# Kernel optimization log

Measured on AMD Instinct MI355X. Metric: run time of the kernel, lower is better.

The kernel has to match this reference:

```python
import jax, jax.numpy as jnp
import numpy as np

NQ, NT, NA = 10000, 50000, 50000
E_GR, E_LT, E_SIM, E_COMP, E_GEN = 50000, 50000, 80000, 100000, 50000
HID, NH, HC, DOT, NL = 512, 4, 128, 256, 2
NEG_SLOPE = 0.2  # PyG GATv2Conv default negative_slope


def _gatv2(x_src, x_dst, src, dst, Wl, bl, Wr, br, att, bias, n_dst):
    # GATv2: x_j = lin_l(x_src), x_i = lin_r(x_dst); e = att . leaky_relu(x_i + x_j)
    xl = (x_src @ Wl + bl).reshape(-1, NH, HC)   # [Ns,H,C]
    xr = (x_dst @ Wr + br).reshape(-1, NH, HC)   # [Nd,H,C]
    m = jax.nn.leaky_relu(xl[src] + xr[dst], NEG_SLOPE)      # [E,H,C]
    logits = jnp.einsum('ehc,hc->eh', m, att)                # [E,H]
    lmax = jax.lax.stop_gradient(jax.ops.segment_max(logits, dst, num_segments=n_dst))
    lmax = jnp.where(jnp.isfinite(lmax), lmax, 0.0)
    ex = jnp.exp(logits - lmax[dst])
    denom = jax.ops.segment_sum(ex, dst, num_segments=n_dst)
    alpha = ex / (denom[dst] + 1e-16)                        # softmax over incoming edges
    out = jax.ops.segment_sum(xl[src] * alpha[:, :, None], dst, num_segments=n_dst)
    return out.reshape(n_dst, NH * HC) + bias


def _layernorm(x, g, b):
    mu = x.mean(-1, keepdims=True)
    var = ((x - mu) ** 2).mean(-1, keepdims=True)
    return (x - mu) / jnp.sqrt(var + 1e-5) * g + b


def _forward(xq, xt, xa, answer_features,
             qp_W, qp_b, tp_W, tp_b, ap_W, ap_b,
             afp_W1, afp_b1, afp_W2, afp_b2,
             conv_Wl, conv_bl, conv_Wr, conv_br, conv_att, conv_bias,
             qh_W, qh_b, qh_g, qh_beta, rh_W, rh_b, rh_g, rh_beta, score_bias,
             ei_gr, ei_lt, ei_sim, ei_comp, ei_gen):
    hq = xq @ qp_W + qp_b
    ht = xt @ tp_W + tp_b
    ha = xa @ ap_W + ap_b
    # add_self_loops=True only for ('query','similar_to','query')
    loops = jnp.arange(NQ, dtype=ei_sim.dtype)
    sim_src = jnp.concatenate([ei_sim[0], loops])
    sim_dst = jnp.concatenate([ei_sim[1], loops])
    for l in range(NL):
        P = lambda r: (conv_Wl[l, r], conv_bl[l, r], conv_Wr[l, r], conv_br[l, r], conv_att[l, r], conv_bias[l, r])
        o_gr = _gatv2(hq, ht, ei_gr[0], ei_gr[1], *P(0), NT)          # query -> think
        o_rgr = _gatv2(ht, hq, ei_gr[1], ei_gr[0], *P(1), NQ)         # think -> query (rev)
        o_lt = _gatv2(ht, ha, ei_lt[0], ei_lt[1], *P(2), NA)          # think -> answer
        o_rlt = _gatv2(ha, ht, ei_lt[1], ei_lt[0], *P(3), NT)         # answer -> think (rev)
        o_sim = _gatv2(hq, hq, sim_src, sim_dst, *P(4), NQ)           # query -> query
        o_cmp = _gatv2(ht, ht, ei_comp[0], ei_comp[1], *P(5), NT)     # think -> think
        # HeteroConv aggr='mean' across relations per destination type, then relu
        hq = jax.nn.relu((o_rgr + o_sim) / 2.0)
        ht = jax.nn.relu((o_gr + o_rlt + o_cmp) / 3.0)
        ha = jax.nn.relu(o_lt)
    q_emb = hq[ei_gen[0]]
    a_emb = ha[ei_gen[1]]
    t_emb = ht[ei_gen[1]]  # faithful to source: think indexed with answer-side index
    af_emb = jax.nn.relu(answer_features @ afp_W1 + afp_b1) @ afp_W2 + afp_b2
    q = _layernorm(q_emb @ qh_W + qh_b, qh_g, qh_beta)
    r = _layernorm(jnp.concatenate([t_emb, a_emb, af_emb], -1) @ rh_W + rh_b, rh_g, rh_beta)
    return (q * r).sum(-1) / jnp.sqrt(jnp.float32(DOT)) + score_bias


def setup_inputs() -> dict:
    ks = jax.random.split(jax.random.key(0), 40)
    n = lambda j, shape, s=0.05: jax.random.normal(ks[j], shape, jnp.float32) * s
    ri = lambda j, shape, hi: jax.random.randint(ks[j], shape, 0, hi, jnp.int32)
    return dict(
        xq=n(0, (NQ, 384), 1.0), xt=n(1, (NT, 384), 1.0), xa=n(2, (NA, 384), 1.0),
        answer_features=n(3, (E_GEN, 6), 1.0),
        qp_W=n(4, (384, HID)), qp_b=n(5, (HID,)),
        tp_W=n(6, (384, HID)), tp_b=n(7, (HID,)),
        ap_W=n(8, (384, HID)), ap_b=n(9, (HID,)),
        afp_W1=n(10, (6, 64)), afp_b1=n(11, (64,)),
        afp_W2=n(12, (64, HID)), afp_b2=n(13, (HID,)),
        conv_Wl=n(14, (NL, 6, HID, HID)), conv_bl=n(15, (NL, 6, HID)),
        conv_Wr=n(16, (NL, 6, HID, HID)), conv_br=n(17, (NL, 6, HID)),
        conv_att=n(18, (NL, 6, NH, HC)), conv_bias=n(19, (NL, 6, HID)),
        qh_W=n(20, (HID, DOT)), qh_b=n(21, (DOT,)),
        qh_g=jnp.ones((DOT,), jnp.float32), qh_beta=jnp.zeros((DOT,), jnp.float32),
        rh_W=n(22, (HID * 3, DOT)), rh_b=n(23, (DOT,)),
        rh_g=jnp.ones((DOT,), jnp.float32), rh_beta=jnp.zeros((DOT,), jnp.float32),
        score_bias=jnp.zeros((1,), jnp.float32),
        ei_gr=jnp.stack([ri(24, (E_GR,), NQ), ri(25, (E_GR,), NT)]),
        ei_lt=jnp.stack([ri(26, (E_LT,), NT), ri(27, (E_LT,), NA)]),
        ei_sim=ri(28, (2, E_SIM), NQ),
        ei_comp=ri(29, (2, E_COMP), NT),
        ei_gen=jnp.stack([ri(30, (E_GEN,), NQ), ri(31, (E_GEN,), NA)]),
    )


def reference(xq, xt, xa, answer_features,
              qp_W, qp_b, tp_W, tp_b, ap_W, ap_b,
              afp_W1, afp_b1, afp_W2, afp_b2,
              conv_Wl, conv_bl, conv_Wr, conv_br, conv_att, conv_bias,
              qh_W, qh_b, qh_g, qh_beta, rh_W, rh_b, rh_g, rh_beta, score_bias,
              ei_gr, ei_lt, ei_sim, ei_comp, ei_gen):
    return _forward(xq, xt, xa, answer_features,
                    qp_W, qp_b, tp_W, tp_b, ap_W, ap_b,
                    afp_W1, afp_b1, afp_W2, afp_b2,
                    conv_Wl, conv_bl, conv_Wr, conv_br, conv_att, conv_bias,
                    qh_W, qh_b, qh_g, qh_beta, rh_W, rh_b, rh_g, rh_beta, score_bias,
                    ei_gr, ei_lt, ei_sim, ei_comp, ei_gen)
```

## Files before the change

### kernel.cpp

```cpp
#include <hip/hip_runtime.h>
#include <cstdio>
#include <type_traits>

#define NQ 10000
#define NT 50000
#define NA 50000
#define E_GR 50000
#define E_LT 50000
#define E_SIM 80000
#define E_COMP 100000
#define E_GEN 50000
#define NEG_SLOPE 0.2f

#define NDTOT 220000
#define NSTOT 220000
#define ETOT  390000
__device__ __constant__ const int c_degOff[7]  = {0, 50000, 60000, 110000, 120000, 170000, 220000};
__device__ __constant__ const int c_sOff[7]    = {0, 10000, 60000, 110000, 120000, 170000, 220000};
__device__ __constant__ const int c_eOff[7]    = {0, 50000, 100000, 150000, 240000, 340000, 390000};
__device__ __constant__ const int c_nb[6]      = {49, 10, 49, 10, 49, 49};
__device__ __constant__ const int c_nbOff[7]   = {0, 49, 59, 108, 118, 167, 216};
__device__ __constant__ const int c_snb[6]     = {10, 49, 49, 10, 49, 49};
__device__ __constant__ const int c_snbOff[7]  = {0, 10, 59, 108, 118, 167, 216};

typedef unsigned short bf16_t;
typedef unsigned int u32;
typedef __attribute__((ext_vector_type(8))) short short8v;
typedef __attribute__((ext_vector_type(4))) float f32x4;

__device__ __forceinline__ float bf2f(u32 bits) { return __uint_as_float(bits << 16); }
__device__ __forceinline__ u32 f2bf(float f) {
  u32 u = __float_as_uint(f);
  return (u + 0x7FFFu + ((u >> 16) & 1u)) >> 16;
}
__device__ __forceinline__ u32 pack2(float a, float b) { return f2bf(a) | (f2bf(b) << 16); }
__device__ __forceinline__ void unpack8(uint4 u, float* f) {
  f[0] = bf2f(u.x & 0xffffu); f[1] = bf2f(u.x >> 16);
  f[2] = bf2f(u.y & 0xffffu); f[3] = bf2f(u.y >> 16);
  f[4] = bf2f(u.z & 0xffffu); f[5] = bf2f(u.z >> 16);
  f[6] = bf2f(u.w & 0xffffu); f[7] = bf2f(u.w >> 16);
}

__device__ __forceinline__ void gload16(const void* g, void* l) {
  __builtin_amdgcn_global_load_lds(
      (const __attribute__((address_space(1))) void*)g,
      (__attribute__((address_space(3))) void*)l, 16, 0, 0);
}

template <typename CT>
__global__ __launch_bounds__(512, 4) void bgemm(
    const bf16_t* __restrict__ A0, const bf16_t* __restrict__ Bt0,
    const float* __restrict__ bias0, CT* __restrict__ C0,
    const int* __restrict__ ridx0, int N0, const int* __restrict__ Nc0,
    const bf16_t* __restrict__ A1, const bf16_t* __restrict__ Bt1,
    const float* __restrict__ bias1, CT* __restrict__ C1,
    const int* __restrict__ ridx1, int N1, const int* __restrict__ Nc1,
    int K, int M, int accumulate)
{
  __shared__ short lds[3][12288];
  const int z = blockIdx.z;
  const bf16_t* A   = z ? A1 : A0;
  const bf16_t* Bt  = z ? Bt1 : Bt0;
  const float* bias = z ? bias1 : bias0;
  CT* C             = z ? C1 : C0;
  const int* ridx   = z ? ridx1 : ridx0;
  const int* Nc     = z ? Nc1 : Nc0;
  int N             = z ? N1 : N0;
  if (Nc) N = *Nc;

  const int tid = threadIdx.x;
  const int ncol = gridDim.x;
  const int nband = (N + 127) >> 7;
  int lin = blockIdx.y * ncol + blockIdx.x;
  if (lin >= ncol * nband) return;

  int band, col;
  const int full = (nband >> 3) * 8 * ncol;
  if (lin < full) {
    int g = lin >> 3, x = lin & 7;
    band = x + 8 * (g / ncol);
    col  = g % ncol;
  } else {
    int r = lin - full;
    band = (nband & ~7) + r / ncol;
    col  = r % ncol;
  }
  const int bm = band * 128, bn = col * 256;

  const int lane = tid & 63;
  const int w = tid >> 6;
  const int wr = w >> 2, wc = w & 3;
  const int fr = lane & 15, fg = lane >> 4;

  const int kg = (((tid & 3) ^ ((tid >> 3) & 3)) << 3);
  const int rr = tid >> 2;
  int ra = min(bm + rr, N - 1);
  const bf16_t* gA0 = A + (size_t)(ridx ? ridx[ra] : ra) * K + kg;
  const bf16_t* gB0 = Bt + (size_t)(bn + rr) * K + kg;
  const bf16_t* gB1 = Bt + (size_t)(bn + 128 + rr) * K + kg;
  const int wb = w << 9;

  f32x4 acc[4][4];
#pragma unroll
  for (int i = 0; i < 4; ++i)
#pragma unroll
    for (int j = 0; j < 4; ++j) acc[i][j] = (f32x4){0.f, 0.f, 0.f, 0.f};

  auto stage = [&](int buf, int k0) {
    short* base = &lds[buf][0];
    gload16(gA0 + k0, base + wb);
    gload16(gB0 + k0, base + 4096 + wb);
    gload16(gB1 + k0, base + 8192 + wb);
  };

  const int nsteps = K >> 5;
  stage(0, 0);
  const int co = (fg ^ ((fr >> 1) & 3)) << 3;
  for (int s = 0; s < nsteps; ++s) {
    const int cur = s % 3;
    if (s + 1 < nsteps) {
      stage((s + 1) % 3, (s + 1) << 5);
      asm volatile("s_waitcnt vmcnt(3)" ::: "memory");
    } else {
      asm volatile("s_waitcnt vmcnt(0)" ::: "memory");
    }
    __builtin_amdgcn_s_barrier();
    asm volatile("" ::: "memory");
    const short* LA = &lds[cur][0];
    const short* LB = &lds[cur][4096];
    short8v b[4];
#pragma unroll
    for (int j = 0; j < 4; ++j) {
      int R = wc * 64 + j * 16 + fr;
      b[j] = *(const short8v*)&LB[R * 32 + co];
    }
#pragma unroll
    for (int i = 0; i < 4; ++i) {
      int R = wr * 64 + i * 16 + fr;
      short8v a = *(const short8v*)&LA[R * 32 + co];
#pragma unroll
      for (int j = 0; j < 4; ++j)
        acc[i][j] = __builtin_amdgcn_mfma_f32_16x16x32_bf16(b[j], a,
                                                            acc[i][j], 0, 0, 0);
    }
    asm volatile("" ::: "memory");
  }

  float4 bv[4];
#pragma unroll
  for (int j = 0; j < 4; ++j) {
    bv[j] = make_float4(0.f, 0.f, 0.f, 0.f);
    if (!accumulate && bias)
      bv[j] = *(const float4*)(bias + bn + wc * 64 + j * 16 + fg * 4);
  }
#pragma unroll
  for (int i = 0; i < 4; ++i) {
    const int n = bm + wr * 64 + i * 16 + fr;
    if (n >= N) continue;
#pragma unroll
    for (int j = 0; j < 4; ++j) {
      const int m0 = bn + wc * 64 + j * 16 + fg * 4;
      f32x4 v = acc[i][j];
      if constexpr (std::is_same<CT, float>::value) {
        float* p = C + (size_t)n * M + m0;
        if (accumulate) {
          float4 o = *(float4*)p;
          o.x += v[0]; o.y += v[1]; o.z += v[2]; o.w += v[3];
          *(float4*)p = o;
        } else {
          *(float4*)p = make_float4(v[0] + bv[j].x, v[1] + bv[j].y,
                                    v[2] + bv[j].z, v[3] + bv[j].w);
        }
      } else {
        uint2 o;
        o.x = pack2(v[0] + bv[j].x, v[1] + bv[j].y);
        o.y = pack2(v[2] + bv[j].z, v[3] + bv[j].w);
        *(uint2*)(C + (size_t)n * M + m0) = o;
      }
    }
  }
}

__device__ __forceinline__ void wT_tile(
    const float* __restrict__ W, bf16_t* __restrict__ Wt, int K, int M)
{
  __shared__ float sm[32][33];
  int mb = blockIdx.x * 32, kb = blockIdx.y * 32;
  int tx = threadIdx.x & 31, ty = threadIdx.x >> 5;
#pragma unroll
  for (int i = 0; i < 4; ++i)
    sm[ty + i * 8][tx] = W[(size_t)(kb + ty + i * 8) * M + mb + tx];
  __syncthreads();
#pragma unroll
  for (int i = 0; i < 4; ++i)
    Wt[(size_t)(mb + ty + i * 8) * K + kb + tx] = (bf16_t)f2bf(sm[tx][ty + i * 8]);
}

__global__ __launch_bounds__(256) void convert_wT(
    const float* __restrict__ W, bf16_t* __restrict__ Wt, int K, int M)
{
  wT_tile(W + (size_t)blockIdx.z * K * M, Wt + (size_t)blockIdx.z * K * M, K, M);
}
__global__ __launch_bounds__(256) void convert_wT24(
    const float* __restrict__ Wl, bf16_t* __restrict__ wl,
    const float* __restrict__ Wr, bf16_t* __restrict__ wr)
{
  int z = blockIdx.z;
  size_t o = (size_t)(z < 12 ? z : z - 12) * 512 * 512;
  if (z < 12) wT_tile(Wl + o, wl + o, 512, 512);
  else        wT_tile(Wr + o, wr + o, 512, 512);
}
__global__ __launch_bounds__(256) void convert_wT3(
    const float* __restrict__ W0, const float* __restrict__ W1,
    const float* __restrict__ W2, bf16_t* __restrict__ T0,
    bf16_t* __restrict__ T1, bf16_t* __restrict__ T2)
{
  int z = blockIdx.z;
  const float* W = z == 0 ? W0 : z == 1 ? W1 : W2;
  bf16_t* T = z == 0 ? T0 : z == 1 ? T1 : T2;
  wT_tile(W, T, 384, 512);
}
__global__ __launch_bounds__(256) void convert_wT4h(
    const float* __restrict__ qh, const float* __restrict__ rh,
    bf16_t* __restrict__ wqh, bf16_t* __restrict__ wrh)
{
  int z = blockIdx.z;
  if (z == 0) wT_tile(qh, wqh, 512, 256);
  else        wT_tile(rh + (size_t)(z - 1) * 512 * 256,
                      wrh + (size_t)(z - 1) * 256 * 512, 512, 256);
}

__global__ __launch_bounds__(256) void cast_flat(
    const float* __restrict__ in, bf16_t* __restrict__ out, int n4)
{
  int t = blockIdx.x * 256 + threadIdx.x;
  if (t >= n4) return;
  float4 v = ((const float4*)in)[t];
  uint2 o;
  o.x = pack2(v.x, v.y);
  o.y = pack2(v.z, v.w);
  ((uint2*)out)[t] = o;
}

__global__ __launch_bounds__(256) void fold_cvec(
    const float* __restrict__ b2, const float* __restrict__ rh2,
    float* __restrict__ cvec)
{
  int m = threadIdx.x;
  float s = 0.f;
  for (int k = 0; k < 512; ++k) s = fmaf(b2[k], rh2[(size_t)k * 256 + m], s);
  cvec[m] = s;
}

#define N4_XQ (NQ * 96)
#define N4_XT (NT * 96)
#define N4_XA (NA * 96)
__global__ __launch_bounds__(256) void cast3(
    const float* __restrict__ xq, const float* __restrict__ xt,
    const float* __restrict__ xa, bf16_t* __restrict__ xqb,
    bf16_t* __restrict__ xtb, bf16_t* __restrict__ xab)
{
  long g = (long)blockIdx.x * 256 + threadIdx.x;
  const float* in; bf16_t* out; long idx;
  if (g < N4_XQ)                { in = xq; out = xqb; idx = g; }
  else if (g < N4_XQ + N4_XT)   { in = xt; out = xtb; idx = g - N4_XQ; }
  else if (g < N4_XQ + N4_XT + N4_XA) { in = xa; out = xab; idx = g - N4_XQ - N4_XT; }
  else return;
  float4 v = ((const float4*)in)[idx];
  uint2 o;
  o.x = pack2(v.x, v.y);
  o.y = pack2(v.z, v.w);
  ((uint2*)out)[idx] = o;
}

__global__ __launch_bounds__(256) void combine_bias6(
    const float* __restrict__ cb, float* __restrict__ bcAll)
{
  int g = blockIdx.x * 256 + threadIdx.x;
  if (g >= 6 * 512) return;
  int row = g >> 9, j = g & 511;
  int l = row / 3, kind = row % 3;
  const float* b = cb + (size_t)l * 6 * 512;
  float v;
  if (kind == 0)      v = (b[0 * 512 + j] + b[3 * 512 + j] + b[5 * 512 + j]) / 3.f;
  else if (kind == 1) v = (b[1 * 512 + j] + b[4 * 512 + j]) * 0.5f;
  else                v = b[2 * 512 + j];
  bcAll[(size_t)row * 512 + j] = v;
}

__device__ __forceinline__ int find_rel6(int g, const int* off) {
  int r = 0;
#pragma unroll
  for (int k = 1; k < 6; ++k) r += (g >= off[k]);
  return r;
}

__global__ __launch_bounds__(256) void hist6(
    const int* __restrict__ d0, const int* __restrict__ d1,
    const int* __restrict__ d2, const int* __restrict__ d3,
    const int* __restrict__ d4, const int* __restrict__ d5,
    const int* __restrict__ s0p, const int* __restrict__ s1p,
    const int* __restrict__ s2p, const int* __restrict__ s3p,
    const int* __restrict__ s4p, const int* __restrict__ s5p,
    int* __restrict__ degAll, int* __restrict__ sdegAll, int* __restrict__ pos)
{
  int g = blockIdx.x * 256 + threadIdx.x;
  if (g >= ETOT) return;
  int r = find_rel6(g, c_eOff);
  int le = g - c_eOff[r];
  const int* dp = r == 0 ? d0 : r == 1 ? d1 : r == 2 ? d2 : r == 3 ? d3
                : r == 4 ? d4 : d5;
  const int* sp = r == 0 ? s0p : r == 1 ? s1p : r == 2 ? s2p : r == 3 ? s3p
                : r == 4 ? s4p : s5p;
  pos[g] = atomicAdd(&degAll[c_degOff[r] + dp[le]], 1);
  atomicAdd(&sdegAll[c_sOff[r] + sp[le]], 1);
}

template <int PRED, int SRC>
__global__ __launch_bounds__(256) void scan1_6(
    const int* __restrict__ in, int* __restrict__ out, int* __restrict__ bsum)
{
  __shared__ int sm[256];
  int b = blockIdx.x;
  const int* nbOff = SRC ? c_snbOff : c_nbOff;
  const int* dOff  = SRC ? c_sOff : c_degOff;
  int r = 0;
#pragma unroll
  for (int k = 1; k < 6; ++k) r += (b >= nbOff[k]);
  int lb = b - nbOff[r];
  int base0 = dOff[r], n = dOff[r + 1] - base0;
  int t = threadIdx.x;
  int base = lb * 1024 + t * 4;
  int v[4], sum = 0;
#pragma unroll
  for (int k = 0; k < 4; ++k) {
    int raw = (base + k < n) ? in[base0 + base + k] : 0;
    v[k] = PRED == 0 ? raw : PRED == 1 ? (raw >= 2 ? 1 : 0) : (raw >= 1 ? 1 : 0);
    sum += v[k];
  }
  sm[t] = sum;
  __syncthreads();
  for (int off = 1; off < 256; off <<= 1) {
    int x = (t >= off) ? sm[t - off] : 0;
    __syncthreads();
    sm[t] += x;
    __syncthreads();
  }
  int run = (t > 0) ? sm[t - 1] : 0;
  if (t == 255) bsum[r * 64 + lb] = sm[255];
#pragma unroll
  for (int k = 0; k < 4; ++k) {
    if (base + k < n) out[base0 + base + k] = run;
    run += v[k];
  }
}

template <int SRC>
__global__ __launch_bounds__(64) void scan2_6(
    int* __restrict__ bsum, int* __restrict__ total)
{
  __shared__ int sm[64];
  int r = blockIdx.x;
  int nb = SRC ? c_snb[r] : c_nb[r];
  int t = threadIdx.x;
  int v = (t < nb) ? bsum[r * 64 + t] : 0;
  sm[t] = v;
  __syncthreads();
  for (int off = 1; off < 64; off <<= 1) {
    int x = (t >= off) ? sm[t - off] : 0;
    __syncthreads();
    sm[t] += x;
    __syncthreads();
  }
  if (t < nb) bsum[r * 64 + t] = sm[t] - v;
  if (total && t == nb - 1) total[r] = sm[t];
}

template <int SRC>
__global__ __launch_bounds__(256) void scan3_6(
    int* __restrict__ out, const int* __restrict__ bsum)
{
  int g = blockIdx.x * 256 + threadIdx.x;
  if (g >= (SRC ? NSTOT : NDTOT)) return;
  const int* dOff = SRC ? c_sOff : c_degOff;
  int r = find_rel6(g, dOff);
  int ln = g - dOff[r];
  out[g] += bsum[r * 64 + (ln >> 10)];
}

__global__ __launch_bounds__(256) void scatter6(
    const int* __restrict__ d0, const int* __restrict__ d1,
    const int* __restrict__ d2, const int* __restrict__ d3,
    const int* __restrict__ d4, const int* __restrict__ d5,
    const int* __restrict__ s0p, const int* __restrict__ s1p,
    const int* __restrict__ s2p, const int* __restrict__ s3p,
    const int* __restrict__ s4p, const int* __restrict__ s5p,
    const int* __restrict__ startAll, const int* __restrict__ pos,
    const int* __restrict__ sposAll,
    int* __restrict__ eidxAll, int* __restrict__ srcCAll)
{
  int g = blockIdx.x * 256 + threadIdx.x;
  if (g >= ETOT) return;
  int r = find_rel6(g, c_eOff);
  int le = g - c_eOff[r];
  const int* dp = r == 0 ? d0 : r == 1 ? d1 : r == 2 ? d2 : r == 3 ? d3
                : r == 4 ? d4 : d5;
  const int* sp = r == 0 ? s0p : r == 1 ? s1p : r == 2 ? s2p : r == 3 ? s3p
                : r == 4 ? s4p : s5p;
  eidxAll[c_eOff[r] + startAll[c_degOff[r] + dp[le]] + pos[g]] = le;
  srcCAll[g] = sposAll[c_sOff[r] + sp[le]];
}

template <int SRC, int THR>
__global__ __launch_bounds__(256) void compact6(
    const int* __restrict__ degA, const int* __restrict__ cposA,
    int* __restrict__ cidxA)
{
  int g = blockIdx.x * 256 + threadIdx.x;
  if (g >= (SRC ? NSTOT : NDTOT)) return;
  if (degA[g] >= THR) {
    const int* dOff = SRC ? c_sOff : c_degOff;
    int r = find_rel6(g, dOff);
    cidxA[dOff[r] + cposA[g]] = g - dOff[r];
  }
}

__global__ __launch_bounds__(256) void gat_fused(
    const bf16_t* __restrict__ xl, const bf16_t* __restrict__ xr,
    const int* __restrict__ srcC, const int* __restrict__ start,
    const int* __restrict__ deg, const int* __restrict__ eidx,
    const int* __restrict__ cpos, const float* __restrict__ att,
    bf16_t* __restrict__ acc, int Nd, int accumulate,
    const float* __restrict__ bc, float inv_div)
{
  int d = blockIdx.x * 4 + (threadIdx.x >> 6);
  if (d >= Nd) return;
  int lane = threadIdx.x & 63;

  float acc8[8] = {0.f, 0.f, 0.f, 0.f, 0.f, 0.f, 0.f, 0.f};
  int n = deg[d], s0 = start[d];
  if (n == 1) {
    int s = srcC[eidx[s0]];
    unpack8(*(const uint4*)(xl + (size_t)s * 512 + lane * 8), acc8);
  } else if (n > 1) {
    float xrr[8];
    unpack8(*(const uint4*)(xr + (size_t)cpos[d] * 512 + lane * 8), xrr);
    float at[8];
    *(float4*)(at)     = *(const float4*)(att + lane * 8);
    *(float4*)(at + 4) = *(const float4*)(att + lane * 8 + 4);
    float den = 0.f;
    int sN = srcC[eidx[s0]];
    for (int i = 0; i < n; ++i) {
      int s = sN;
      if (i + 1 < n) sN = srcC[eidx[s0 + i + 1]];
      float f[8];
      unpack8(*(const uint4*)(xl + (size_t)s * 512 + lane * 8), f);
      float p = 0.f;
#pragma unroll
      for (int k = 0; k < 8; ++k) {
        float x = f[k] + xrr[k];
        p = fmaf(at[k], x >= 0.f ? x : NEG_SLOPE * x, p);
      }
#pragma unroll
      for (int m = 8; m >= 1; m >>= 1) p += __shfl_xor(p, m);
      float ex = __expf(p);
      den += ex;
#pragma unroll
      for (int k = 0; k < 8; ++k) acc8[k] = fmaf(ex, f[k], acc8[k]);
    }
    float inv = 1.f / (den + 1e-16f);
#pragma unroll
    for (int k = 0; k < 8; ++k) acc8[k] *= inv;
  }

  bf16_t* out = acc + (size_t)d * 512 + lane * 8;
  if (accumulate) {
    float old[8];
    unpack8(*(const uint4*)out, old);
#pragma unroll
    for (int k = 0; k < 8; ++k) acc8[k] += old[k];
  }
  if (bc) {
    float bcv[8];
    *(float4*)(bcv)     = *(const float4*)(bc + lane * 8);
    *(float4*)(bcv + 4) = *(const float4*)(bc + lane * 8 + 4);
#pragma unroll
    for (int k = 0; k < 8; ++k)
      acc8[k] = fmaxf(fmaf(acc8[k], inv_div, bcv[k]), 0.f);
  }
  uint4 s;
  s.x = pack2(acc8[0], acc8[1]); s.y = pack2(acc8[2], acc8[3]);
  s.z = pack2(acc8[4], acc8[5]); s.w = pack2(acc8[6], acc8[7]);
  *(uint4*)out = s;
}

__global__ __launch_bounds__(256) void af_hidden(
    const float* __restrict__ af, const float* __restrict__ W1,
    const float* __restrict__ b1, bf16_t* __restrict__ out, int n)
{
  int t = blockIdx.x * blockDim.x + threadIdx.x;
  if (t >= n * 64) return;
  int i = t >> 6, j = t & 63;
  const float* a = af + (size_t)i * 6;
  float s = b1[j];
#pragma unroll
  for (int k = 0; k < 6; ++k) s = fmaf(a[k], W1[k * 64 + j], s);
  out[t] = (bf16_t)f2bf(fmaxf(s, 0.f));
}

__global__ __launch_bounds__(256) void build_sim(
    const int* __restrict__ ei, int* __restrict__ ss, int* __restrict__ sd)
{
  int t = blockIdx.x * blockDim.x + threadIdx.x;
  if (t >= E_SIM + NQ) return;
  if (t < E_SIM) { ss[t] = ei[t]; sd[t] = ei[E_SIM + t]; }
  else           { ss[t] = t - E_SIM; sd[t] = t - E_SIM; }
}

__global__ __launch_bounds__(256) void head_final(
    const float* __restrict__ qn, const float* __restrict__ rn,
    const float* __restrict__ afr, const float* __restrict__ cvec,
    const int* __restrict__ gsrc, const int* __restrict__ gdst,
    const float* __restrict__ qg, const float* __restrict__ qb,
    const float* __restrict__ rg, const float* __restrict__ rb,
    const float* __restrict__ score_bias, float* __restrict__ out, int E)
{
  int e = blockIdx.x * 4 + (threadIdx.x >> 6);
  if (e >= E) return;
  int lane = threadIdx.x & 63;

  float4 q = *(const float4*)(qn + (size_t)gsrc[e] * 256 + lane * 4);
  float s = q.x + q.y + q.z + q.w;
#pragma unroll
  for (int m = 32; m >= 1; m >>= 1) s += __shfl_xor(s, m);
  float mu = s * (1.f / 256.f);
  float dq0 = q.x - mu, dq1 = q.y - mu, dq2 = q.z - mu, dq3 = q.w - mu;
  float v = dq0 * dq0 + dq1 * dq1 + dq2 * dq2 + dq3 * dq3;
#pragma unroll
  for (int m = 32; m >= 1; m >>= 1) v += __shfl_xor(v, m);
  float rstd = rsqrtf(v * (1.f / 256.f) + 1e-5f);
  float4 g4 = *(const float4*)(qg + lane * 4);
  float4 b4 = *(const float4*)(qb + lane * 4);
  float qn0 = dq0 * rstd * g4.x + b4.x, qn1 = dq1 * rstd * g4.y + b4.y;
  float qn2 = dq2 * rstd * g4.z + b4.z, qn3 = dq3 * rstd * g4.w + b4.w;

  float4 r0 = *(const float4*)(rn + (size_t)gdst[e] * 256 + lane * 4);
  float4 r1 = *(const float4*)(afr + (size_t)e * 256 + lane * 4);
  float4 cv = *(const float4*)(cvec + lane * 4);
  float4 r;
  r.x = r0.x + r1.x + cv.x;
  r.y = r0.y + r1.y + cv.y;
  r.z = r0.z + r1.z + cv.z;
  r.w = r0.w + r1.w + cv.w;
  s = r.x + r.y + r.z + r.w;
#pragma unroll
  for (int m = 32; m >= 1; m >>= 1) s += __shfl_xor(s, m);
  mu = s * (1.f / 256.f);
  float dr0 = r.x - mu, dr1 = r.y - mu, dr2 = r.z - mu, dr3 = r.w - mu;
  v = dr0 * dr0 + dr1 * dr1 + dr2 * dr2 + dr3 * dr3;
#pragma unroll
  for (int m = 32; m >= 1; m >>= 1) v += __shfl_xor(v, m);
  rstd = rsqrtf(v * (1.f / 256.f) + 1e-5f);
  g4 = *(const float4*)(rg + lane * 4);
  b4 = *(const float4*)(rb + lane * 4);
  float rn0 = dr0 * rstd * g4.x + b4.x, rn1 = dr1 * rstd * g4.y + b4.y;
  float rn2 = dr2 * rstd * g4.z + b4.z, rn3 = dr3 * rstd * g4.w + b4.w;

  float d = qn0 * rn0 + qn1 * rn1 + qn2 * rn2 + qn3 * rn3;
#pragma unroll
  for (int m = 32; m >= 1; m >>= 1) d += __shfl_xor(d, m);
  if (lane == 0) out[e] = d * 0.0625f + score_bias[0];
}

extern "C" void kernel_launch(void* const* d_in, const int* in_sizes, int n_in,
                              void* d_out, int out_size, void* d_ws, size_t ws_size,
                              hipStream_t stream) {
  (void)in_sizes; (void)n_in; (void)out_size;
  const float* xq      = (const float*)d_in[0];
  const float* xt      = (const float*)d_in[1];
  const float* xa      = (const float*)d_in[2];
  const float* af      = (const float*)d_in[3];
  const float* qp_W    = (const float*)d_in[4];
  const float* qp_b    = (const float*)d_in[5];
  const float* tp_W    = (const float*)d_in[6];
  const float* tp_b    = (const float*)d_in[7];
  const float* ap_W    = (const float*)d_in[8];
  const float* ap_b    = (const float*)d_in[9];
  const float* afp_W1  = (const float*)d_in[10];
  const float* afp_b1  = (const float*)d_in[11];
  const float* afp_W2  = (const float*)d_in[12];
  const float* afp_b2  = (const float*)d_in[13];
  const float* conv_Wl = (const float*)d_in[14];
  const float* conv_bl = (const float*)d_in[15];
  const float* conv_Wr = (const float*)d_in[16];
  const float* conv_br = (const float*)d_in[17];
  const float* conv_att  = (const float*)d_in[18];
  const float* conv_bias = (const float*)d_in[19];
  const float* qh_W    = (const float*)d_in[20];
  const float* qh_b    = (const float*)d_in[21];
  const float* qh_g    = (const float*)d_in[22];
  const float* qh_beta = (const float*)d_in[23];
  const float* rh_W    = (const float*)d_in[24];
  const float* rh_b    = (const float*)d_in[25];
  const float* rh_g    = (const float*)d_in[26];
  const float* rh_beta = (const float*)d_in[27];
  const float* score_b = (const float*)d_in[28];
  const int* ei_gr   = (const int*)d_in[29];
  const int* ei_lt   = (const int*)d_in[30];
  const int* ei_sim  = (const int*)d_in[31];
  const int* ei_comp = (const int*)d_in[32];
  const int* ei_gen  = (const int*)d_in[33];

  char* base = (char*)d_ws;
  size_t off = 0;
  auto alloc = [&](size_t bytes) {
    void* p = base + off;
    off = (off + bytes + 255) & ~(size_t)255;
    return p;
  };
  bf16_t* hq   = (bf16_t*)alloc((size_t)NQ * 512 * 2);
  bf16_t* ht   = (bf16_t*)alloc((size_t)NT * 512 * 2);
  bf16_t* ha   = (bf16_t*)alloc((size_t)NA * 512 * 2);
  bf16_t* acct = (bf16_t*)alloc((size_t)NT * 512 * 2);
  bf16_t* accq = (bf16_t*)alloc((size_t)NQ * 512 * 2);
  bf16_t* xlb  = (bf16_t*)alloc((size_t)50000 * 512 * 2);
  bf16_t* xrb  = (bf16_t*)alloc((size_t)50000 * 512 * 2);
  int* simsrc  = (int*)alloc((size_t)(E_SIM + NQ) * 4);
  int* simdst  = (int*)alloc((size_t)(E_SIM + NQ) * 4);

  bf16_t* wqp  = (bf16_t*)alloc((size_t)512 * 384 * 2);
  bf16_t* wtp  = (bf16_t*)alloc((size_t)512 * 384 * 2);
  bf16_t* wap  = (bf16_t*)alloc((size_t)512 * 384 * 2);
  bf16_t* wl   = (bf16_t*)alloc((size_t)12 * 512 * 512 * 2);
  bf16_t* wr   = (bf16_t*)alloc((size_t)12 * 512 * 512 * 2);
  bf16_t* wqh  = (bf16_t*)alloc((size_t)256 * 512 * 2);
  bf16_t* wrh0 = (bf16_t*)alloc((size_t)256 * 512 * 2);
  bf16_t* wrh1 = (bf16_t*)alloc((size_t)256 * 512 * 2);
  bf16_t* wrh2 = (bf16_t*)alloc((size_t)256 * 512 * 2);
  float* bcAll = (float*)alloc(6 * 512 * 4);
  bf16_t* a2b    = (bf16_t*)alloc((size_t)64 * 512 * 2);
  float*  wfoldF = (float*)alloc((size_t)64 * 256 * 4);
  bf16_t* wfoldT = (bf16_t*)alloc((size_t)256 * 64 * 2);
  float*  cvec   = (float*)alloc(256 * 4);

  int* degAll   = (int*)alloc((size_t)NDTOT * 4);
  int* startAll = (int*)alloc((size_t)NDTOT * 4);
  int* cposAll  = (int*)alloc((size_t)NDTOT * 4);
  int* cidxAll  = (int*)alloc((size_t)NDTOT * 4);
  int* sdegAll  = (int*)alloc((size_t)NSTOT * 4);
  int* sposAll  = (int*)alloc((size_t)NSTOT * 4);
  int* sidxAll  = (int*)alloc((size_t)NSTOT * 4);
  int* eidxAll  = (int*)alloc((size_t)ETOT * 4);
  int* srcCAll  = (int*)alloc((size_t)ETOT * 4);
  int* posb     = (int*)alloc((size_t)ETOT * 4);
  int* bsum     = (int*)alloc(6 * 64 * 4);
  int* bsum2    = (int*)alloc(6 * 64 * 4);
  int* sbsum    = (int*)alloc(6 * 64 * 4);
  int* ccount   = (int*)alloc(6 * 4);
  int* scount   = (int*)alloc(6 * 4);
  if (off > ws_size) {
    fprintf(stderr, "kernel_launch: ws too small, need %zu have %zu\n", off, ws_size);
    return;
  }

  const int degOff[6] = {0, 50000, 60000, 110000, 120000, 170000};
  const int sOff[6]   = {0, 10000, 60000, 110000, 120000, 170000};
  const int eOff[6]   = {0, 50000, 100000, 150000, 240000, 340000};

  auto gemm1 = [&](const bf16_t* A, const bf16_t* Bt, const float* bias, bf16_t* C,
                   int N_, int K_, int M_, const int* ridx = nullptr) {
    dim3 g(M_ / 256, (N_ + 127) / 128, 1);
    bgemm<bf16_t><<<g, 512, 0, stream>>>(A, Bt, bias, C, ridx, N_, nullptr,
                                         A, Bt, bias, C, ridx, N_, nullptr,
                                         K_, M_, 0);
  };
  auto gemmf1 = [&](const bf16_t* A, const bf16_t* Bt, const float* bias, float* C,
                    int N_, int K_, int M_, int acc_, const int* ridx = nullptr) {
    dim3 g(M_ / 256, (N_ + 127) / 128, 1);
    bgemm<float><<<g, 512, 0, stream>>>(A, Bt, bias, C, ridx, N_, nullptr,
                                        A, Bt, bias, C, ridx, N_, nullptr,
                                        K_, M_, acc_);
  };
  auto gemm2 = [&](const bf16_t* A0, const bf16_t* B0, const float* b0, bf16_t* C0, int N0_,
                   const bf16_t* A1, const bf16_t* B1, const float* b1, bf16_t* C1, int N1_,
                   int K_, int M_) {
    int nb0 = (N0_ + 127) / 128, nb1 = (N1_ + 127) / 128;
    dim3 g(M_ / 256, nb0 > nb1 ? nb0 : nb1, 2);
    bgemm<bf16_t><<<g, 512, 0, stream>>>(A0, B0, b0, C0, nullptr, N0_, nullptr,
                                         A1, B1, b1, C1, nullptr, N1_, nullptr,
                                         K_, M_, 0);
  };
  auto gemm2cc = [&](const bf16_t* A0, const bf16_t* B0, const float* b0, bf16_t* C0,
                     const int* sidx, int N0max, const int* Ns_,
                     const bf16_t* A1, const bf16_t* B1, const float* b1, bf16_t* C1,
                     const int* cidx, int N1max, const int* Ncnt) {
    int nb0 = (N0max + 127) / 128, nb1 = (N1max + 127) / 128;
    dim3 g(2, nb0 > nb1 ? nb0 : nb1, 2);
    bgemm<bf16_t><<<g, 512, 0, stream>>>(A0, B0, b0, C0, sidx, N0max, Ns_,
                                         A1, B1, b1, C1, cidx, N1max, Ncnt,
                                         512, 512, 0);
  };
  auto gemmf2 = [&](const bf16_t* A0, const bf16_t* B0, const float* b0, float* C0, int N0_,
                    const bf16_t* A1, const bf16_t* B1, const float* b1, float* C1, int N1_,
                    int K_, int M_) {
    int nb0 = (N0_ + 127) / 128, nb1 = (N1_ + 127) / 128;
    dim3 g(M_ / 256, nb0 > nb1 ? nb0 : nb1, 2);
    bgemm<float><<<g, 512, 0, stream>>>(A0, B0, b0, C0, nullptr, N0_, nullptr,
                                        A1, B1, b1, C1, nullptr, N1_, nullptr,
                                        K_, M_, 0);
  };

  convert_wT24<<<dim3(16, 16, 24), 256, 0, stream>>>(conv_Wl, wl, conv_Wr, wr);
  convert_wT3<<<dim3(16, 12, 3), 256, 0, stream>>>(qp_W, tp_W, ap_W, wqp, wtp, wap);
  convert_wT4h<<<dim3(8, 16, 4), 256, 0, stream>>>(qh_W, rh_W, wqh, wrh0);
  combine_bias6<<<(6 * 512 + 255) / 256, 256, 0, stream>>>(conv_bias, bcAll);
  cast_flat<<<(64 * 512 / 4 + 255) / 256, 256, 0, stream>>>(afp_W2, a2b, 64 * 512 / 4);
  gemmf1(a2b, wrh2, nullptr, wfoldF, 64, 512, 256, 0);
  convert_wT<<<dim3(8, 2, 1), 256, 0, stream>>>(wfoldF, wfoldT, 64, 256);
  fold_cvec<<<1, 256, 0, stream>>>(afp_b2, rh_W + 1024 * 256, cvec);

  build_sim<<<(E_SIM + NQ + 255) / 256, 256, 0, stream>>>(ei_sim, simsrc, simdst);
  const int* dsts[6]  = {ei_gr + E_GR, ei_gr, ei_lt, simdst,
                         ei_comp + E_COMP, ei_lt + E_LT};
  const int* srcsA[6] = {ei_gr, ei_gr + E_GR, ei_lt + E_LT, simsrc,
                         ei_comp, ei_lt};
  hipMemsetAsync(degAll, 0, (size_t)NDTOT * 4, stream);
  hipMemsetAsync(sdegAll, 0, (size_t)NSTOT * 4, stream);
  hist6<<<(ETOT + 255) / 256, 256, 0, stream>>>(
      dsts[0], dsts[1], dsts[2], dsts[3], dsts[4], dsts[5],
      srcsA[0], srcsA[1], srcsA[2], srcsA[3], srcsA[4], srcsA[5],
      degAll, sdegAll, posb);
  scan1_6<0, 0><<<216, 256, 0, stream>>>(degAll, startAll, bsum);
  scan1_6<1, 0><<<216, 256, 0, stream>>>(degAll, cposAll, bsum2);
  scan1_6<2, 1><<<216, 256, 0, stream>>>(sdegAll, sposAll, sbsum);
  scan2_6<0><<<6, 64, 0, stream>>>(bsum, nullptr);
  scan2_6<0><<<6, 64, 0, stream>>>(bsum2, ccount);
  scan2_6<1><<<6, 64, 0, stream>>>(sbsum, scount);
  scan3_6<0><<<(NDTOT + 255) / 256, 256, 0, stream>>>(startAll, bsum);
  scan3_6<0><<<(NDTOT + 255) / 256, 256, 0, stream>>>(cposAll, bsum2);
  scan3_6<1><<<(NSTOT + 255) / 256, 256, 0, stream>>>(sposAll, sbsum);
  scatter6<<<(ETOT + 255) / 256, 256, 0, stream>>>(
      dsts[0], dsts[1], dsts[2], dsts[3], dsts[4], dsts[5],
      srcsA[0], srcsA[1], srcsA[2], srcsA[3], srcsA[4], srcsA[5],
      startAll, posb, sposAll, eidxAll, srcCAll);
  compact6<0, 2><<<(NDTOT + 255) / 256, 256, 0, stream>>>(degAll, cposAll, cidxAll);
  compact6<1, 1><<<(NSTOT + 255) / 256, 256, 0, stream>>>(sdegAll, sposAll, sidxAll);

  cast3<<<((long)(N4_XQ + N4_XT + N4_XA) + 255) / 256, 256, 0, stream>>>(
      xq, xt, xa, accq, xlb, xrb);
  gemm1(accq, wqp, qp_b, hq, NQ, 384, 512);
  gemm2(xlb, wtp, tp_b, ht, NT, xrb, wap, ap_b, ha, NA, 384, 512);

  const int NdArr[6] = {NT, NQ, NT, NQ, NT, NA};
  const int NsArr[6] = {NQ, NT, NA, NQ, NT, NT};
  bf16_t *hq_i = hq, *ht_i = ht, *hq_o = accq, *ht_o = acct;
  for (int l = 0; l < 2; ++l) {
    const float* bc_t = bcAll + (size_t)(l * 3 + 0) * 512;
    const float* bc_q = bcAll + (size_t)(l * 3 + 1) * 512;
    const float* bc_a = bcAll + (size_t)(l * 3 + 2) * 512;

    struct Rel { const bf16_t* xs; const bf16_t* xd; int po; bf16_t* acc;
                 int accum; const float* bc; float inv; };
    Rel rels[6] = {
      {hq_i, ht_i, 0, ht_o, 0, nullptr, 0.f},
      {ht_i, hq_i, 1, hq_o, 0, nullptr, 0.f},
      {ha,   ht_i, 3, ht_o, 1, nullptr, 0.f},
      {hq_i, hq_i, 4, hq_o, 1, bc_q, 0.5f},
      {ht_i, ht_i, 5, ht_o, 1, bc_t, 1.f / 3.f},
      {ht_i, ha,   2, ha,   0, bc_a, 1.f},
    };
    for (int r = 0; r < 6; ++r) {
      const Rel& R = rels[r];
      int Nd_ = NdArr[r];
      size_t po = (size_t)l * 6 + R.po;
      gemm2cc(R.xs, wl + po * 512 * 512, conv_bl + po * 512, xlb,
              sidxAll + sOff[r], NsArr[r], scount + r,
              R.xd, wr + po * 512 * 512, conv_br + po * 512, xrb,
              cidxAll + degOff[r], Nd_, ccount + r);
      int gb = (Nd_ + 3) / 4;
      gat_fused<<<gb, 256, 0, stream>>>(xlb, xrb, srcCAll + eOff[r],
                                        startAll + degOff[r], degAll + degOff[r],
                                        eidxAll + eOff[r], cposAll + degOff[r],
                                        conv_att + po * 512,
                                        R.acc, Nd_, R.accum, R.bc, R.inv);
    }
    bf16_t* t;
    t = hq_i; hq_i = hq_o; hq_o = t;
    t = ht_i; ht_i = ht_o; ht_o = t;
  }

  float* qn  = (float*)accq;
  float* rn  = (float*)acct;
  float* afr = (float*)xrb;
  bf16_t* afh = xlb;
  const int* gsrc = ei_gen;
  const int* gdst = ei_gen + E_GEN;

  gemmf2(hq_i, wqh, qh_b, qn, NQ, ht_i, wrh0, rh_b, rn, NT, 512, 256);
  gemmf1(ha, wrh1, nullptr, rn, NA, 512, 256, 1);
  af_hidden<<<(E_GEN * 64 + 255) / 256, 256, 0, stream>>>(af, afp_W1, afp_b1,
                                                          afh, E_GEN);
  gemmf1(afh, wfoldT, nullptr, afr, E_GEN, 64, 256, 0);
  head_final<<<(E_GEN + 3) / 4, 256, 0, stream>>>(
      qn, rn, afr, cvec, gsrc, gdst,
      qh_g, qh_beta, rh_g, rh_beta, score_b, (float*)d_out, E_GEN);
}
```

Before: 1.207 ms.

## Cut kernel launches: single-pass scans, merged compaction, batched GEMMs

The three-kernel block scans are replaced by one kernel of 18 blocks, each scanning a whole relation segment serially with a running carry. The two compaction kernels become one, the two degree memsets become one, and the GEMM kernel now takes up to three descriptors so that the projection GEMMs and the head GEMMs are batched into fewer launches. The goal is to cut launch count and small-kernel overhead. The cost is a long serial scan in only 18 blocks, which may take longer than the parallel version for segments of 50k elements.

New measurement: 1.255 ms. 1.04x slower.

```diff
diff --git a/kernel.cpp b/kernel.cpp
--- a/kernel.cpp
+++ b/kernel.cpp
@@ -18,10 +18,6 @@
 __device__ __constant__ const int c_degOff[7]  = {0, 50000, 60000, 110000, 120000, 170000, 220000};
 __device__ __constant__ const int c_sOff[7]    = {0, 10000, 60000, 110000, 120000, 170000, 220000};
 __device__ __constant__ const int c_eOff[7]    = {0, 50000, 100000, 150000, 240000, 340000, 390000};
-__device__ __constant__ const int c_nb[6]      = {49, 10, 49, 10, 49, 49};
-__device__ __constant__ const int c_nbOff[7]   = {0, 49, 59, 108, 118, 167, 216};
-__device__ __constant__ const int c_snb[6]     = {10, 49, 49, 10, 49, 49};
-__device__ __constant__ const int c_snbOff[7]  = {0, 10, 59, 108, 118, 167, 216};
 
 typedef unsigned short bf16_t;
 typedef unsigned int u32;
@@ -47,26 +43,20 @@
       (__attribute__((address_space(3))) void*)l, 16, 0, 0);
 }
 
+struct GemmDesc {
+  const bf16_t* A; const bf16_t* Bt; const float* bias; void* C;
+  const int* ridx; int N; const int* Nc; int K;
+};
+
 template <typename CT>
 __global__ __launch_bounds__(512, 4) void bgemm(
-    const bf16_t* __restrict__ A0, const bf16_t* __restrict__ Bt0,
-    const float* __restrict__ bias0, CT* __restrict__ C0,
-    const int* __restrict__ ridx0, int N0, const int* __restrict__ Nc0,
-    const bf16_t* __restrict__ A1, const bf16_t* __restrict__ Bt1,
-    const float* __restrict__ bias1, CT* __restrict__ C1,
-    const int* __restrict__ ridx1, int N1, const int* __restrict__ Nc1,
-    int K, int M, int accumulate)
+    GemmDesc d0, GemmDesc d1, GemmDesc d2, int M, int accumulate)
 {
   __shared__ short lds[3][12288];
   const int z = blockIdx.z;
-  const bf16_t* A   = z ? A1 : A0;
-  const bf16_t* Bt  = z ? Bt1 : Bt0;
-  const float* bias = z ? bias1 : bias0;
-  CT* C             = z ? C1 : C0;
-  const int* ridx   = z ? ridx1 : ridx0;
-  const int* Nc     = z ? Nc1 : Nc0;
-  int N             = z ? N1 : N0;
-  if (Nc) N = *Nc;
+  GemmDesc d = (z == 2) ? d2 : (z == 1) ? d1 : d0;
+  int N = d.Nc ? *d.Nc : d.N;
+  const int K = d.K;
 
   const int tid = threadIdx.x;
   const int ncol = gridDim.x;
@@ -95,9 +85,9 @@
   const int kg = (((tid & 3) ^ ((tid >> 3) & 3)) << 3);
   const int rr = tid >> 2;
   int ra = min(bm + rr, N - 1);
-  const bf16_t* gA0 = A + (size_t)(ridx ? ridx[ra] : ra) * K + kg;
-  const bf16_t* gB0 = Bt + (size_t)(bn + rr) * K + kg;
-  const bf16_t* gB1 = Bt + (size_t)(bn + 128 + rr) * K + kg;
+  const bf16_t* gA0 = d.A + (size_t)(d.ridx ? d.ridx[ra] : ra) * K + kg;
+  const bf16_t* gB0 = d.Bt + (size_t)(bn + rr) * K + kg;
+  const bf16_t* gB1 = d.Bt + (size_t)(bn + 128 + rr) * K + kg;
   const int wb = w << 9;
 
   f32x4 acc[4][4];
@@ -146,12 +136,13 @@
     asm volatile("" ::: "memory");
   }
 
+  CT* C = (CT*)d.C;
   float4 bv[4];
 #pragma unroll
   for (int j = 0; j < 4; ++j) {
     bv[j] = make_float4(0.f, 0.f, 0.f, 0.f);
-    if (!accumulate && bias)
-      bv[j] = *(const float4*)(bias + bn + wc * 64 + j * 16 + fg * 4);
+    if (!accumulate && d.bias)
+      bv[j] = *(const float4*)(d.bias + bn + wc * 64 + j * 16 + fg * 4);
   }
 #pragma unroll
   for (int i = 0; i < 4; ++i) {
@@ -316,76 +307,50 @@
   atomicAdd(&sdegAll[c_sOff[r] + sp[le]], 1);
 }
 
-template <int PRED, int SRC>
-__global__ __launch_bounds__(256) void scan1_6(
-    const int* __restrict__ in, int* __restrict__ out, int* __restrict__ bsum)
+__global__ __launch_bounds__(256) void scanAll(
+    const int* __restrict__ degAll, const int* __restrict__ sdegAll,
+    int* __restrict__ startAll, int* __restrict__ cposAll,
+    int* __restrict__ sposAll, int* __restrict__ ccount, int* __restrict__ scount)
 {
   __shared__ int sm[256];
   int b = blockIdx.x;
-  const int* nbOff = SRC ? c_snbOff : c_nbOff;
-  const int* dOff  = SRC ? c_sOff : c_degOff;
-  int r = 0;
-#pragma unroll
-  for (int k = 1; k < 6; ++k) r += (b >= nbOff[k]);
-  int lb = b - nbOff[r];
+  int j = b / 6, r = b % 6;
+  const int* dOff = (j == 2) ? c_sOff : c_degOff;
+  const int* in   = (j == 2) ? sdegAll : degAll;
+  int* out = j == 0 ? startAll : j == 1 ? cposAll : sposAll;
   int base0 = dOff[r], n = dOff[r + 1] - base0;
   int t = threadIdx.x;
-  int base = lb * 1024 + t * 4;
-  int v[4], sum = 0;
-#pragma unroll
-  for (int k = 0; k < 4; ++k) {
-    int raw = (base + k < n) ? in[base0 + base + k] : 0;
-    v[k] = PRED == 0 ? raw : PRED == 1 ? (raw >= 2 ? 1 : 0) : (raw >= 1 ? 1 : 0);
-    sum += v[k];
-  }
-  sm[t] = sum;
-  __syncthreads();
-  for (int off = 1; off < 256; off <<= 1) {
-    int x = (t >= off) ? sm[t - off] : 0;
+  int carry = 0;
+  for (int c0 = 0; c0 < n; c0 += 1024) {
+    int base = c0 + t * 4;
+    int v[4], sum = 0;
+#pragma unroll
+    for (int k = 0; k < 4; ++k) {
+      int raw = (base + k < n) ? in[base0 + base + k] : 0;
+      v[k] = j == 0 ? raw : j == 1 ? (raw >= 2 ? 1 : 0) : (raw >= 1 ? 1 : 0);
+      sum += v[k];
+    }
+    sm[t] = sum;
     __syncthreads();
-    sm[t] += x;
+    for (int off = 1; off < 256; off <<= 1) {
+      int x = (t >= off) ? sm[t - off] : 0;
+      __syncthreads();
+      sm[t] += x;
+      __syncthreads();
+    }
+    int run = carry + (t > 0 ? sm[t - 1] : 0);
+#pragma unroll
+    for (int k = 0; k < 4; ++k) {
+      if (base + k < n) out[base0 + base + k] = run;
+      run += v[k];
+    }
+    carry += sm[255];
     __syncthreads();
   }
-  int run = (t > 0) ? sm[t - 1] : 0;
-  if (t == 255) bsum[r * 64 + lb] = sm[255];
-#pragma unroll
-  for (int k = 0; k < 4; ++k) {
-    if (base + k < n) out[base0 + base + k] = run;
-    run += v[k];
-  }
-}
-
-template <int SRC>
-__global__ __launch_bounds__(64) void scan2_6(
-    int* __restrict__ bsum, int* __restrict__ total)
-{
-  __shared__ int sm[64];
-  int r = blockIdx.x;
-  int nb = SRC ? c_snb[r] : c_nb[r];
-  int t = threadIdx.x;
-  int v = (t < nb) ? bsum[r * 64 + t] : 0;
-  sm[t] = v;
-  __syncthreads();
-  for (int off = 1; off < 64; off <<= 1) {
-    int x = (t >= off) ? sm[t - off] : 0;
-    __syncthreads();
-    sm[t] += x;
-    __syncthreads();
-  }
-  if (t < nb) bsum[r * 64 + t] = sm[t] - v;
-  if (total && t == nb - 1) total[r] = sm[t];
-}
-
-template <int SRC>
-__global__ __launch_bounds__(256) void scan3_6(
-    int* __restrict__ out, const int* __restrict__ bsum)
-{
-  int g = blockIdx.x * 256 + threadIdx.x;
-  if (g >= (SRC ? NSTOT : NDTOT)) return;
-  const int* dOff = SRC ? c_sOff : c_degOff;
-  int r = find_rel6(g, dOff);
-  int ln = g - dOff[r];
-  out[g] += bsum[r * 64 + (ln >> 10)];
+  if (t == 0) {
+    if (j == 1) ccount[r] = carry;
+    if (j == 2) scount[r] = carry;
+  }
 }
 
 __global__ __launch_bounds__(256) void scatter6(
@@ -411,17 +376,24 @@
   srcCAll[g] = sposAll[c_sOff[r] + sp[le]];
 }
 
-template <int SRC, int THR>
-__global__ __launch_bounds__(256) void compact6(
-    const int* __restrict__ degA, const int* __restrict__ cposA,
-    int* __restrict__ cidxA)
+__global__ __launch_bounds__(256) void compactBoth(
+    const int* __restrict__ degAll, const int* __restrict__ cposAll,
+    int* __restrict__ cidxAll,
+    const int* __restrict__ sdegAll, const int* __restrict__ sposAll,
+    int* __restrict__ sidxAll)
 {
   int g = blockIdx.x * 256 + threadIdx.x;
-  if (g >= (SRC ? NSTOT : NDTOT)) return;
-  if (degA[g] >= THR) {
-    const int* dOff = SRC ? c_sOff : c_degOff;
-    int r = find_rel6(g, dOff);
-    cidxA[dOff[r] + cposA[g]] = g - dOff[r];
+  if (g < NDTOT) {
+    if (degAll[g] >= 2) {
+      int r = find_rel6(g, c_degOff);
+      cidxAll[c_degOff[r] + cposAll[g]] = g - c_degOff[r];
+    }
+  } else if (g < NDTOT + NSTOT) {
+    int h = g - NDTOT;
+    if (sdegAll[h] >= 1) {
+      int r = find_rel6(h, c_sOff);
+      sidxAll[c_sOff[r] + sposAll[h]] = h - c_sOff[r];
+    }
   }
 }
 
@@ -644,18 +616,15 @@
   float*  cvec   = (float*)alloc(256 * 4);
 
   int* degAll   = (int*)alloc((size_t)NDTOT * 4);
+  int* sdegAll  = (int*)alloc((size_t)NSTOT * 4);
   int* startAll = (int*)alloc((size_t)NDTOT * 4);
   int* cposAll  = (int*)alloc((size_t)NDTOT * 4);
   int* cidxAll  = (int*)alloc((size_t)NDTOT * 4);
-  int* sdegAll  = (int*)alloc((size_t)NSTOT * 4);
   int* sposAll  = (int*)alloc((size_t)NSTOT * 4);
   int* sidxAll  = (int*)alloc((size_t)NSTOT * 4);
   int* eidxAll  = (int*)alloc((size_t)ETOT * 4);
   int* srcCAll  = (int*)alloc((size_t)ETOT * 4);
   int* posb     = (int*)alloc((size_t)ETOT * 4);
-  int* bsum     = (int*)alloc(6 * 64 * 4);
-  int* bsum2    = (int*)alloc(6 * 64 * 4);
-  int* sbsum    = (int*)alloc(6 * 64 * 4);
   int* ccount   = (int*)alloc(6 * 4);
   int* scount   = (int*)alloc(6 * 4);
   if (off > ws_size) {
@@ -667,47 +636,22 @@
   const int sOff[6]   = {0, 10000, 60000, 110000, 120000, 170000};
   const int eOff[6]   = {0, 50000, 100000, 150000, 240000, 340000};
 
-  auto gemm1 = [&](const bf16_t* A, const bf16_t* Bt, const float* bias, bf16_t* C,
-                   int N_, int K_, int M_, const int* ridx = nullptr) {
-    dim3 g(M_ / 256, (N_ + 127) / 128, 1);
-    bgemm<bf16_t><<<g, 512, 0, stream>>>(A, Bt, bias, C, ridx, N_, nullptr,
-                                         A, Bt, bias, C, ridx, N_, nullptr,
-                                         K_, M_, 0);
+  auto mkDesc = [](const bf16_t* A, const bf16_t* Bt, const float* bias, void* C,
+                   const int* ridx, int N, const int* Nc, int K) {
+    GemmDesc d; d.A = A; d.Bt = Bt; d.bias = bias; d.C = C;
+    d.ridx = ridx; d.N = N; d.Nc = Nc; d.K = K; return d;
   };
-  auto gemmf1 = [&](const bf16_t* A, const bf16_t* Bt, const float* bias, float* C,
-                    int N_, int K_, int M_, int acc_, const int* ridx = nullptr) {
-    dim3 g(M_ / 256, (N_ + 127) / 128, 1);
-    bgemm<float><<<g, 512, 0, stream>>>(A, Bt, bias, C, ridx, N_, nullptr,
-                                        A, Bt, bias, C, ridx, N_, nullptr,
-                                        K_, M_, acc_);
+  GemmDesc dz = mkDesc(nullptr, nullptr, nullptr, nullptr, nullptr, 0, nullptr, 32);
+
+  auto launch_b = [&](GemmDesc a, GemmDesc b, GemmDesc c, int nz, int maxN,
+                      int M, int acc_) {
+    dim3 g(M / 256, (maxN + 127) / 128, nz);
+    bgemm<bf16_t><<<g, 512, 0, stream>>>(a, b, c, M, acc_);
   };
-  auto gemm2 = [&](const bf16_t* A0, const bf16_t* B0, const float* b0, bf16_t* C0, int N0_,
-                   const bf16_t* A1, const bf16_t* B1, const float* b1, bf16_t* C1, int N1_,
-                   int K_, int M_) {
-    int nb0 = (N0_ + 127) / 128, nb1 = (N1_ + 127) / 128;
-    dim3 g(M_ / 256, nb0 > nb1 ? nb0 : nb1, 2);
-    bgemm<bf16_t><<<g, 512, 0, stream>>>(A0, B0, b0, C0, nullptr, N0_, nullptr,
-                                         A1, B1, b1, C1, nullptr, N1_, nullptr,
-                                         K_, M_, 0);
-  };
-  auto gemm2cc = [&](const bf16_t* A0, const bf16_t* B0, const float* b0, bf16_t* C0,
-                     const int* sidx, int N0max, const int* Ns_,
-                     const bf16_t* A1, const bf16_t* B1, const float* b1, bf16_t* C1,
-                     const int* cidx, int N1max, const int* Ncnt) {
-    int nb0 = (N0max + 127) / 128, nb1 = (N1max + 127) / 128;
-    dim3 g(2, nb0 > nb1 ? nb0 : nb1, 2);
-    bgemm<bf16_t><<<g, 512, 0, stream>>>(A0, B0, b0, C0, sidx, N0max, Ns_,
-                                         A1, B1, b1, C1, cidx, N1max, Ncnt,
-                                         512, 512, 0);
-  };
-  auto gemmf2 = [&](const bf16_t* A0, const bf16_t* B0, const float* b0, float* C0, int N0_,
-                    const bf16_t* A1, const bf16_t* B1, const float* b1, float* C1, int N1_,
-                    int K_, int M_) {
-    int nb0 = (N0_ + 127) / 128, nb1 = (N1_ + 127) / 128;
-    dim3 g(M_ / 256, nb0 > nb1 ? nb0 : nb1, 2);
-    bgemm<float><<<g, 512, 0, stream>>>(A0, B0, b0, C0, nullptr, N0_, nullptr,
-                                        A1, B1, b1, C1, nullptr, N1_, nullptr,
-                                        K_, M_, 0);
+  auto launch_f = [&](GemmDesc a, GemmDesc b, GemmDesc c, int nz, int maxN,
+                      int M, int acc_) {
+    dim3 g(M / 256, (maxN + 127) / 128, nz);
+    bgemm<float><<<g, 512, 0, stream>>>(a, b, c, M, acc_);
   };
 
   convert_wT24<<<dim3(16, 16, 24), 256, 0, stream>>>(conv_Wl, wl, conv_Wr, wr);
@@ -715,7 +659,8 @@
   convert_wT4h<<<dim3(8, 16, 4), 256, 0, stream>>>(qh_W, rh_W, wqh, wrh0);
   combine_bias6<<<(6 * 512 + 255) / 256, 256, 0, stream>>>(conv_bias, bcAll);
   cast_flat<<<(64 * 512 / 4 + 255) / 256, 256, 0, stream>>>(afp_W2, a2b, 64 * 512 / 4);
-  gemmf1(a2b, wrh2, nullptr, wfoldF, 64, 512, 256, 0);
+  launch_f(mkDesc(a2b, wrh2, nullptr, wfoldF, nullptr, 64, nullptr, 512),
+           dz, dz, 1, 64, 256, 0);
   convert_wT<<<dim3(8, 2, 1), 256, 0, stream>>>(wfoldF, wfoldT, 64, 256);
   fold_cvec<<<1, 256, 0, stream>>>(afp_b2, rh_W + 1024 * 256, cvec);
 
@@ -724,32 +669,26 @@
                          ei_comp + E_COMP, ei_lt + E_LT};
   const int* srcsA[6] = {ei_gr, ei_gr + E_GR, ei_lt + E_LT, simsrc,
                          ei_comp, ei_lt};
-  hipMemsetAsync(degAll, 0, (size_t)NDTOT * 4, stream);
-  hipMemsetAsync(sdegAll, 0, (size_t)NSTOT * 4, stream);
+  hipMemsetAsync(degAll, 0, (size_t)(sdegAll + NSTOT) - (size_t)degAll, stream);
   hist6<<<(ETOT + 255) / 256, 256, 0, stream>>>(
       dsts[0], dsts[1], dsts[2], dsts[3], dsts[4], dsts[5],
       srcsA[0], srcsA[1], srcsA[2], srcsA[3], srcsA[4], srcsA[5],
       degAll, sdegAll, posb);
-  scan1_6<0, 0><<<216, 256, 0, stream>>>(degAll, startAll, bsum);
-  scan1_6<1, 0><<<216, 256, 0, stream>>>(degAll, cposAll, bsum2);
-  scan1_6<2, 1><<<216, 256, 0, stream>>>(sdegAll, sposAll, sbsum);
-  scan2_6<0><<<6, 64, 0, stream>>>(bsum, nullptr);
-  scan2_6<0><<<6, 64, 0, stream>>>(bsum2, ccount);
-  scan2_6<1><<<6, 64, 0, stream>>>(sbsum, scount);
-  scan3_6<0><<<(NDTOT + 255) / 256, 256, 0, stream>>>(startAll, bsum);
-  scan3_6<0><<<(NDTOT + 255) / 256, 256, 0, stream>>>(cposAll, bsum2);
-  scan3_6<1><<<(NSTOT + 255) / 256, 256, 0, stream>>>(sposAll, sbsum);
+  scanAll<<<18, 256, 0, stream>>>(degAll, sdegAll, startAll, cposAll, sposAll,
+                                  ccount, scount);
   scatter6<<<(ETOT + 255) / 256, 256, 0, stream>>>(
       dsts[0], dsts[1], dsts[2], dsts[3], dsts[4], dsts[5],
       srcsA[0], srcsA[1], srcsA[2], srcsA[3], srcsA[4], srcsA[5],
       startAll, posb, sposAll, eidxAll, srcCAll);
-  compact6<0, 2><<<(NDTOT + 255) / 256, 256, 0, stream>>>(degAll, cposAll, cidxAll);
-  compact6<1, 1><<<(NSTOT + 255) / 256, 256, 0, stream>>>(sdegAll, sposAll, sidxAll);
+  compactBoth<<<(NDTOT + NSTOT + 255) / 256, 256, 0, stream>>>(
+      degAll, cposAll, cidxAll, sdegAll, sposAll, sidxAll);
 
   cast3<<<((long)(N4_XQ + N4_XT + N4_XA) + 255) / 256, 256, 0, stream>>>(
       xq, xt, xa, accq, xlb, xrb);
-  gemm1(accq, wqp, qp_b, hq, NQ, 384, 512);
-  gemm2(xlb, wtp, tp_b, ht, NT, xrb, wap, ap_b, ha, NA, 384, 512);
+  launch_b(mkDesc(accq, wqp, qp_b, hq, nullptr, NQ, nullptr, 384),
+           mkDesc(xlb, wtp, tp_b, ht, nullptr, NT, nullptr, 384),
+           mkDesc(xrb, wap, ap_b, ha, nullptr, NA, nullptr, 384),
+           3, NT, 512, 0);
 
   const int NdArr[6] = {NT, NQ, NT, NQ, NT, NA};
   const int NsArr[6] = {NQ, NT, NA, NQ, NT, NT};
@@ -773,10 +712,12 @@
       const Rel& R = rels[r];
       int Nd_ = NdArr[r];
       size_t po = (size_t)l * 6 + R.po;
-      gemm2cc(R.xs, wl + po * 512 * 512, conv_bl + po * 512, xlb,
-              sidxAll + sOff[r], NsArr[r], scount + r,
-              R.xd, wr + po * 512 * 512, conv_br + po * 512, xrb,
-              cidxAll + degOff[r], Nd_, ccount + r);
+      int maxN = NsArr[r] > Nd_ ? NsArr[r] : Nd_;
+      launch_b(mkDesc(R.xs, wl + po * 512 * 512, conv_bl + po * 512, xlb,
+                      sidxAll + sOff[r], NsArr[r], scount + r, 512),
+               mkDesc(R.xd, wr + po * 512 * 512, conv_br + po * 512, xrb,
+                      cidxAll + degOff[r], Nd_, ccount + r, 512),
+               dz, 2, maxN, 512, 0);
       int gb = (Nd_ + 3) / 4;
       gat_fused<<<gb, 256, 0, stream>>>(xlb, xrb, srcCAll + eOff[r],
                                         startAll + degOff[r], degAll + degOff[r],
@@ -796,11 +737,14 @@
   const int* gsrc = ei_gen;
   const int* gdst = ei_gen + E_GEN;
 
-  gemmf2(hq_i, wqh, qh_b, qn, NQ, ht_i, wrh0, rh_b, rn, NT, 512, 256);
-  gemmf1(ha, wrh1, nullptr, rn, NA, 512, 256, 1);
   af_hidden<<<(E_GEN * 64 + 255) / 256, 256, 0, stream>>>(af, afp_W1, afp_b1,
                                                           afh, E_GEN);
-  gemmf1(afh, wfoldT, nullptr, afr, E_GEN, 64, 256, 0);
+  launch_f(mkDesc(hq_i, wqh, qh_b, qn, nullptr, NQ, nullptr, 512),
+           mkDesc(ht_i, wrh0, rh_b, rn, nullptr, NT, nullptr, 512),
+           mkDesc(afh, wfoldT, nullptr, afr, nullptr, E_GEN, nullptr, 64),
+           3, NT, 256, 0);
+  launch_f(mkDesc(ha, wrh1, nullptr, rn, nullptr, NA, nullptr, 512),
+           dz, dz, 1, NA, 256, 1);
   head_final<<<(E_GEN + 3) / 4, 256, 0, stream>>>(
       qn, rn, afr, cvec, gsrc, gdst,
       qh_g, qh_beta, rh_g, rh_beta, score_b, (float*)d_out, E_GEN);
```
